# Kernel optimization log

Hardware: AMD Instinct MI355X
Metric: run time of the kernel (lower is better)

Reference implementation:

```python
import jax, jax.numpy as jnp
import numpy as np

N_USER = 100000
N_ITEM = 50000
D = 128
E = 600000
LN_EPS = 1e-5
NEG_SLOPE = 0.01  # torch nn.LeakyReLU default


def setup_inputs() -> dict:
    key = jax.random.key(0)
    ks = jax.random.split(key, 8)
    scale = 1.0 / np.sqrt(D)
    return {
        "x_user": jax.random.normal(ks[0], (N_USER, D), jnp.float32),
        "x_item": jax.random.normal(ks[1], (N_ITEM, D), jnp.float32),
        "W_ui": jax.random.normal(ks[2], (D, D), jnp.float32) * scale,
        "b_ui": jnp.zeros((D,), jnp.float32),
        "W_iu": jax.random.normal(ks[3], (D, D), jnp.float32) * scale,
        "b_iu": jnp.zeros((D,), jnp.float32),
        "ln_w_user": jnp.ones((D,), jnp.float32),
        "ln_b_user": jnp.zeros((D,), jnp.float32),
        "ln_w_item": jnp.ones((D,), jnp.float32),
        "ln_b_item": jnp.zeros((D,), jnp.float32),
        "edge_src_ui": jax.random.randint(ks[4], (E,), 0, N_USER, jnp.int32),
        "edge_dst_ui": jax.random.randint(ks[5], (E,), 0, N_ITEM, jnp.int32),
        "edge_src_iu": jax.random.randint(ks[6], (E,), 0, N_ITEM, jnp.int32),
        "edge_dst_iu": jax.random.randint(ks[7], (E,), 0, N_USER, jnp.int32),
    }


def _ngcf_conv(x_src, x_dst, W, b, src_idx, dst_idx, num_dst):
    # message: LeakyReLU(Linear(x_j * x_i)) per edge, then scatter-add at dst
    m = jax.nn.leaky_relu((x_src[src_idx] * x_dst[dst_idx]) @ W + b, NEG_SLOPE)
    return jax.ops.segment_sum(m, dst_idx, num_segments=num_dst)


def _node_layernorm(x, w, b):
    # PyG LayerNorm(mode='node'): normalize each node over feature dim
    mu = jnp.mean(x, axis=-1, keepdims=True)
    var = jnp.mean(jnp.square(x - mu), axis=-1, keepdims=True)
    return (x - mu) * jax.lax.rsqrt(var + LN_EPS) * w + b


def reference(x_user, x_item, W_ui, b_ui, W_iu, b_iu,
              ln_w_user, ln_b_user, ln_w_item, ln_b_item,
              edge_src_ui, edge_dst_ui, edge_src_iu, edge_dst_iu):
    # HeteroConv with aggr='sum' (single relation per destination type here)
    agg_item = _ngcf_conv(x_user, x_item, W_ui, b_ui, edge_src_ui, edge_dst_ui, N_ITEM)
    agg_user = _ngcf_conv(x_item, x_user, W_iu, b_iu, edge_src_iu, edge_dst_iu, N_USER)
    out_user = jax.nn.relu(_node_layernorm(agg_user, ln_w_user, ln_b_user))
    out_item = jax.nn.relu(_node_layernorm(agg_item, ln_w_item, ln_b_item))
    return out_user, out_item
```

## Files before the change

kernel.cpp:

```cpp
#include <hip/hip_runtime.h>
#include <stdint.h>

#define D 128
#define E_EDGES 600000
#define N_USER_C 100000
#define N_ITEM_C 50000
#define NEG_SLOPE 0.01f
#define LN_EPS 1e-5f

#define LDPAD 136
#define GRID_BLOCKS 1024
#define GRID_WAVES (GRID_BLOCKS * 4)

typedef __attribute__((ext_vector_type(8))) short bf16x8;
typedef __attribute__((ext_vector_type(4))) float f32x4;
typedef __attribute__((ext_vector_type(4))) uint32_t u32x4;

__device__ inline short f2bf(float f) {
    uint32_t u = __builtin_bit_cast(uint32_t, f);
    u += 0x7fffu + ((u >> 16) & 1u);
    return (short)(u >> 16);
}
__device__ inline uint32_t pack2f(float a, float b) {
    return (uint32_t)(uint16_t)f2bf(a) | ((uint32_t)(uint16_t)f2bf(b) << 16);
}


__global__ void hist_k(const int* __restrict__ dst, int* __restrict__ counts, int n) {
    int e = blockIdx.x * 256 + threadIdx.x;
    if (e < n) atomicAdd(&counts[dst[e]], 1);
}

__global__ void scan_block_k(const int* __restrict__ counts, int* __restrict__ offsets,
                             int* __restrict__ partial, int n) {
    __shared__ int sm[1024];
    const int t = threadIdx.x;
    const int i = blockIdx.x * 1024 + t;
    int v = (i < n) ? counts[i] : 0;
    sm[t] = v;
    __syncthreads();
    for (int off = 1; off < 1024; off <<= 1) {
        int x = (t >= off) ? sm[t - off] : 0;
        __syncthreads();
        sm[t] += x;
        __syncthreads();
    }
    if (i < n) offsets[i] = sm[t] - v;
    if (t == 1023) partial[blockIdx.x] = sm[t];
}

__global__ void scan_part_k(int* __restrict__ partial, int nb) {
    __shared__ int sm[128];
    const int t = threadIdx.x;
    int v = (t < nb) ? partial[t] : 0;
    sm[t] = v;
    __syncthreads();
    for (int off = 1; off < 128; off <<= 1) {
        int x = (t >= off) ? sm[t - off] : 0;
        __syncthreads();
        sm[t] += x;
        __syncthreads();
    }
    if (t < nb) partial[t] = sm[t] - v;
}

__global__ void scan_add_k(int* __restrict__ offsets, const int* __restrict__ partial,
                           int* __restrict__ counts, int n) {
    const int i = blockIdx.x * 1024 + threadIdx.x;
    if (i < n) {
        offsets[i] += partial[blockIdx.x];
        counts[i] = 0;
    }
}

__global__ void scatter_k(const int* __restrict__ src, const int* __restrict__ dst,
                          const int* __restrict__ offsets, int* __restrict__ counts,
                          int* __restrict__ sorted, int n) {
    int e = blockIdx.x * 256 + threadIdx.x;
    if (e < n) {
        int d = dst[e];
        int pos = offsets[d] + atomicAdd(&counts[d], 1);
        sorted[pos] = src[e];
    }
}

__global__ __launch_bounds__(256, 2) void ngcf_seg(
    const float* __restrict__ xsrc, const float* __restrict__ xdst,
    const float* __restrict__ W, const float* __restrict__ bias,
    const int* __restrict__ offsets, const int* __restrict__ sorted,
    const float* __restrict__ lnw, const float* __restrict__ lnb,
    float* __restrict__ outp, int n_dst, int n_edges)
{
    __shared__ short Wt[128 * LDPAD];

    const int t = threadIdx.x;
    for (int i = t; i < 128 * 128; i += 256) {
        int k = i >> 7, n = i & 127;
        Wt[n * LDPAD + k] = f2bf(W[i]);
    }
    __syncthreads();

    const int wv   = t >> 6;
    const int l    = t & 63;
    const int lo16 = l & 15;
    const int quad = l >> 4;

    float bn[8];
    #pragma unroll
    for (int n = 0; n < 8; n++) bn[n] = bias[n * 16 + lo16];

    for (int d = blockIdx.x * 4 + wv; d < n_dst; d += GRID_WAVES) {
        const int start = offsets[d];
        const int end   = (d + 1 < n_dst) ? offsets[d + 1] : n_edges;
        const int len   = end - start;

        const float4* pd = (const float4*)(xdst + ((size_t)d << 7));
        float4 dr[8];
        #pragma unroll
        for (int kt = 0; kt < 4; kt++) {
            dr[kt * 2 + 0] = pd[kt * 8 + quad * 2 + 0];
            dr[kt * 2 + 1] = pd[kt * 8 + quad * 2 + 1];
        }

        float nacc[8];
        #pragma unroll
        for (int n = 0; n < 8; n++) nacc[n] = 0.f;

        for (int c0 = 0; c0 < len; c0 += 16) {
            const int eidx = c0 + lo16;
            const int si = (eidx < len) ? sorted[start + eidx] : 0;
            const float4* ps = (const float4*)(xsrc + ((size_t)si << 7));

            f32x4 acc[8];
            #pragma unroll
            for (int n = 0; n < 8; n++) acc[n] = (f32x4){0.f, 0.f, 0.f, 0.f};

            #pragma unroll
            for (int kt = 0; kt < 4; kt++) {
                float4 a0 = ps[kt * 8 + quad * 2 + 0];
                float4 a1 = ps[kt * 8 + quad * 2 + 1];
                float4 c0v = dr[kt * 2 + 0];
                float4 c1v = dr[kt * 2 + 1];
                u32x4 up;
                up[0] = pack2f(a0.x * c0v.x, a0.y * c0v.y);
                up[1] = pack2f(a0.z * c0v.z, a0.w * c0v.w);
                up[2] = pack2f(a1.x * c1v.x, a1.y * c1v.y);
                up[3] = pack2f(a1.z * c1v.z, a1.w * c1v.w);
                bf16x8 afrag = __builtin_bit_cast(bf16x8, up);
                #pragma unroll
                for (int n = 0; n < 8; n++) {
                    bf16x8 bfrag = *(const bf16x8*)&Wt[(n * 16 + lo16) * LDPAD + kt * 32 + quad * 8];
                    acc[n] = __builtin_amdgcn_mfma_f32_16x16x32_bf16(afrag, bfrag, acc[n], 0, 0, 0);
                }
            }

            const int rem = len - c0;
            #pragma unroll
            for (int r = 0; r < 4; r++) {
                const bool ok = (quad * 4 + r) < rem;
                #pragma unroll
                for (int n = 0; n < 8; n++) {
                    float v = acc[n][r] + bn[n];
                    v = v > 0.f ? v : NEG_SLOPE * v;
                    nacc[n] += ok ? v : 0.f;
                }
            }
        }

        #pragma unroll
        for (int n = 0; n < 8; n++) {
            nacc[n] += __shfl_xor(nacc[n], 16);
            nacc[n] += __shfl_xor(nacc[n], 32);
        }

        float s1 = 0.f, s2 = 0.f;
        #pragma unroll
        for (int n = 0; n < 8; n++) { s1 += nacc[n]; s2 += nacc[n] * nacc[n]; }
        #pragma unroll
        for (int off = 1; off <= 8; off <<= 1) {
            s1 += __shfl_xor(s1, off);
            s2 += __shfl_xor(s2, off);
        }
        const float mu  = s1 * (1.0f / 128.0f);
        const float var = s2 * (1.0f / 128.0f) - mu * mu;
        const float rs  = rsqrtf(var + LN_EPS);

        const int n0 = 2 * quad, n1 = n0 + 1;
        const int col0 = n0 * 16 + lo16, col1 = n1 * 16 + lo16;
        float o0 = (nacc[n0] - mu) * rs * lnw[col0] + lnb[col0];
        float o1 = (nacc[n1] - mu) * rs * lnw[col1] + lnb[col1];
        float* rp = outp + ((size_t)d << 7);
        rp[col0] = fmaxf(o0, 0.f);
        rp[col1] = fmaxf(o1, 0.f);
    }
}


static inline void run_relation(const float* xsrc, const float* xdst,
                                const float* W, const float* bias,
                                const int* src, const int* dst,
                                const float* lnw, const float* lnb,
                                float* outp, int n_dst,
                                int* counts, int* offsets, int* partial, int* sorted,
                                hipStream_t stream) {
    const int nb = (n_dst + 1023) / 1024;
    hipMemsetAsync(counts, 0, (size_t)n_dst * sizeof(int), stream);
    hist_k<<<dim3((E_EDGES + 255) / 256), dim3(256), 0, stream>>>(dst, counts, E_EDGES);
    scan_block_k<<<dim3(nb), dim3(1024), 0, stream>>>(counts, offsets, partial, n_dst);
    scan_part_k<<<dim3(1), dim3(128), 0, stream>>>(partial, nb);
    scan_add_k<<<dim3(nb), dim3(1024), 0, stream>>>(offsets, partial, counts, n_dst);
    scatter_k<<<dim3((E_EDGES + 255) / 256), dim3(256), 0, stream>>>(src, dst, offsets, counts, sorted, E_EDGES);
    ngcf_seg<<<dim3(GRID_BLOCKS), dim3(256), 0, stream>>>(
        xsrc, xdst, W, bias, offsets, sorted, lnw, lnb, outp, n_dst, E_EDGES);
}

extern "C" void kernel_launch(void* const* d_in, const int* in_sizes, int n_in,
                              void* d_out, int out_size, void* d_ws, size_t ws_size,
                              hipStream_t stream) {
    const float* x_user    = (const float*)d_in[0];
    const float* x_item    = (const float*)d_in[1];
    const float* W_ui      = (const float*)d_in[2];
    const float* b_ui      = (const float*)d_in[3];
    const float* W_iu      = (const float*)d_in[4];
    const float* b_iu      = (const float*)d_in[5];
    const float* ln_w_user = (const float*)d_in[6];
    const float* ln_b_user = (const float*)d_in[7];
    const float* ln_w_item = (const float*)d_in[8];
    const float* ln_b_item = (const float*)d_in[9];
    const int* esrc_ui = (const int*)d_in[10];
    const int* edst_ui = (const int*)d_in[11];
    const int* esrc_iu = (const int*)d_in[12];
    const int* edst_iu = (const int*)d_in[13];

    float* out = (float*)d_out;
    float* out_user = out;
    float* out_item = out + (size_t)N_USER_C * D;

    int* counts  = (int*)d_ws;
    int* offsets = counts + 100032;
    int* partial = offsets + 100032;
    int* sorted  = partial + 192;

    run_relation(x_user, x_item, W_ui, b_ui, esrc_ui, edst_ui,
                 ln_w_item, ln_b_item, out_item, N_ITEM_C,
                 counts, offsets, partial, sorted, stream);
    run_relation(x_item, x_user, W_iu, b_iu, esrc_iu, edst_iu,
                 ln_w_user, ln_b_user, out_user, N_USER_C,
                 counts, offsets, partial, sorted, stream);
}
```

Before: 601.1 us.

## Merge both relations into one CSR build and one fused conv launch with fp16 MFMA

Both edge relations now share a single histogram, scan and scatter pass over a combined destination space, and a single conv kernel handles them by splitting blocks on the low bit of the block index. This cuts the launch count roughly in half and lets the two relations run concurrently on the GPU. The MFMA path moves from bf16 to fp16: inputs are converted with packed round-toward-zero and multiplied in fp16. The bias is folded into the accumulator initialisation, and padded lanes read a zero row, with their LeakyReLU(bias) contribution subtracted afterwards instead of masked per element. The fp16 elementwise product and round-toward-zero conversion may change numerical accuracy, and the padded lanes still read sorted[] past the end of a segment.

```diff
diff --git a/kernel.cpp b/kernel.cpp
--- a/kernel.cpp
+++ b/kernel.cpp
@@ -3,32 +3,31 @@
 
 #define D 128
 #define E_EDGES 600000
+#define E2 1200000
 #define N_USER_C 100000
 #define N_ITEM_C 50000
+#define NSEG_TOT 150000
+#define NCPAD 150528
 #define NEG_SLOPE 0.01f
 #define LN_EPS 1e-5f
 
 #define LDPAD 136
 #define GRID_BLOCKS 1024
+#define TOTAL_BLOCKS (GRID_BLOCKS * 2)
 #define GRID_WAVES (GRID_BLOCKS * 4)
 
-typedef __attribute__((ext_vector_type(8))) short bf16x8;
+typedef __attribute__((ext_vector_type(8))) _Float16 f16x8;
+typedef __attribute__((ext_vector_type(2))) _Float16 f16x2;
 typedef __attribute__((ext_vector_type(4))) float f32x4;
+typedef __attribute__((ext_vector_type(2))) float f32x2;
 typedef __attribute__((ext_vector_type(4))) uint32_t u32x4;
 
-__device__ inline short f2bf(float f) {
-    uint32_t u = __builtin_bit_cast(uint32_t, f);
-    u += 0x7fffu + ((u >> 16) & 1u);
-    return (short)(u >> 16);
-}
-__device__ inline uint32_t pack2f(float a, float b) {
-    return (uint32_t)(uint16_t)f2bf(a) | ((uint32_t)(uint16_t)f2bf(b) << 16);
-}
-
-
-__global__ void hist_k(const int* __restrict__ dst, int* __restrict__ counts, int n) {
+
+__global__ void hist2_k(const int* __restrict__ edst_ui, const int* __restrict__ edst_iu,
+                        int* __restrict__ counts) {
     int e = blockIdx.x * 256 + threadIdx.x;
-    if (e < n) atomicAdd(&counts[dst[e]], 1);
+    if (e < E_EDGES) atomicAdd(&counts[edst_ui[e]], 1);
+    else if (e < 2 * E_EDGES) atomicAdd(&counts[N_ITEM_C + edst_iu[e - E_EDGES]], 1);
 }
 
 __global__ void scan_block_k(const int* __restrict__ counts, int* __restrict__ offsets,
@@ -50,12 +49,12 @@
 }
 
 __global__ void scan_part_k(int* __restrict__ partial, int nb) {
-    __shared__ int sm[128];
+    __shared__ int sm[256];
     const int t = threadIdx.x;
     int v = (t < nb) ? partial[t] : 0;
     sm[t] = v;
     __syncthreads();
-    for (int off = 1; off < 128; off <<= 1) {
+    for (int off = 1; off < 256; off <<= 1) {
         int x = (t >= off) ? sm[t - off] : 0;
         __syncthreads();
         sm[t] += x;
@@ -73,30 +72,47 @@
     }
 }
 
-__global__ void scatter_k(const int* __restrict__ src, const int* __restrict__ dst,
-                          const int* __restrict__ offsets, int* __restrict__ counts,
-                          int* __restrict__ sorted, int n) {
+__global__ void scatter2_k(const int* __restrict__ esrc_ui, const int* __restrict__ edst_ui,
+                           const int* __restrict__ esrc_iu, const int* __restrict__ edst_iu,
+                           const int* __restrict__ offsets, int* __restrict__ counts,
+                           int* __restrict__ sorted) {
     int e = blockIdx.x * 256 + threadIdx.x;
-    if (e < n) {
-        int d = dst[e];
-        int pos = offsets[d] + atomicAdd(&counts[d], 1);
-        sorted[pos] = src[e];
-    }
-}
-
-__global__ __launch_bounds__(256, 2) void ngcf_seg(
-    const float* __restrict__ xsrc, const float* __restrict__ xdst,
-    const float* __restrict__ W, const float* __restrict__ bias,
+    int s, c;
+    if (e < E_EDGES)          { s = esrc_ui[e];            c = edst_ui[e]; }
+    else if (e < 2 * E_EDGES) { s = esrc_iu[e - E_EDGES];  c = N_ITEM_C + edst_iu[e - E_EDGES]; }
+    else return;
+    int pos = offsets[c] + atomicAdd(&counts[c], 1);
+    sorted[pos] = s;
+}
+
+__global__ __launch_bounds__(256, 2) void ngcf_seg2(
+    const float* __restrict__ xu, const float* __restrict__ xi,
+    const float* __restrict__ W_ui, const float* __restrict__ b_ui,
+    const float* __restrict__ W_iu, const float* __restrict__ b_iu,
+    const float* __restrict__ lnw_u, const float* __restrict__ lnb_u,
+    const float* __restrict__ lnw_i, const float* __restrict__ lnb_i,
     const int* __restrict__ offsets, const int* __restrict__ sorted,
-    const float* __restrict__ lnw, const float* __restrict__ lnb,
-    float* __restrict__ outp, int n_dst, int n_edges)
+    const float* __restrict__ zrow,
+    float* __restrict__ out_user, float* __restrict__ out_item)
 {
-    __shared__ short Wt[128 * LDPAD];
+    __shared__ _Float16 Wt[128 * LDPAD];
+
+    const int rel = blockIdx.x & 1;
+    const int bid = blockIdx.x >> 1;
+    const float* __restrict__ xsrc = rel ? xi : xu;
+    const float* __restrict__ xdst = rel ? xu : xi;
+    const float* __restrict__ Wp   = rel ? W_iu : W_ui;
+    const float* __restrict__ bp   = rel ? b_iu : b_ui;
+    const float* __restrict__ lnw  = rel ? lnw_u : lnw_i;
+    const float* __restrict__ lnb  = rel ? lnb_u : lnb_i;
+    float* __restrict__ outp       = rel ? out_user : out_item;
+    const int n_dst = rel ? N_USER_C : N_ITEM_C;
+    const int obase = rel ? N_ITEM_C : 0;
 
     const int t = threadIdx.x;
     for (int i = t; i < 128 * 128; i += 256) {
         int k = i >> 7, n = i & 127;
-        Wt[n * LDPAD + k] = f2bf(W[i]);
+        Wt[n * LDPAD + k] = (_Float16)Wp[i];
     }
     __syncthreads();
 
@@ -107,70 +123,78 @@
 
     float bn[8];
     #pragma unroll
-    for (int n = 0; n < 8; n++) bn[n] = bias[n * 16 + lo16];
-
-    for (int d = blockIdx.x * 4 + wv; d < n_dst; d += GRID_WAVES) {
-        const int start = offsets[d];
-        const int end   = (d + 1 < n_dst) ? offsets[d + 1] : n_edges;
+    for (int n = 0; n < 8; n++) bn[n] = bp[n * 16 + lo16];
+
+    for (int d = bid * 4 + wv; d < n_dst; d += GRID_WAVES) {
+        const int start = offsets[obase + d];
+        const int end   = offsets[obase + d + 1];
         const int len   = end - start;
 
         const float4* pd = (const float4*)(xdst + ((size_t)d << 7));
-        float4 dr[8];
+        f16x8 dr[4];
         #pragma unroll
         for (int kt = 0; kt < 4; kt++) {
-            dr[kt * 2 + 0] = pd[kt * 8 + quad * 2 + 0];
-            dr[kt * 2 + 1] = pd[kt * 8 + quad * 2 + 1];
-        }
-
-        float nacc[8];
-        #pragma unroll
-        for (int n = 0; n < 8; n++) nacc[n] = 0.f;
-
-        for (int c0 = 0; c0 < len; c0 += 16) {
-            const int eidx = c0 + lo16;
-            const int si = (eidx < len) ? sorted[start + eidx] : 0;
-            const float4* ps = (const float4*)(xsrc + ((size_t)si << 7));
+            float4 c0 = pd[kt * 8 + quad * 2 + 0];
+            float4 c1 = pd[kt * 8 + quad * 2 + 1];
+            u32x4 u;
+            u[0] = __builtin_bit_cast(uint32_t, __builtin_amdgcn_cvt_pkrtz(c0.x, c0.y));
+            u[1] = __builtin_bit_cast(uint32_t, __builtin_amdgcn_cvt_pkrtz(c0.z, c0.w));
+            u[2] = __builtin_bit_cast(uint32_t, __builtin_amdgcn_cvt_pkrtz(c1.x, c1.y));
+            u[3] = __builtin_bit_cast(uint32_t, __builtin_amdgcn_cvt_pkrtz(c1.z, c1.w));
+            dr[kt] = __builtin_bit_cast(f16x8, u);
+        }
+
+        f32x2 nacc2[8];
+        #pragma unroll
+        for (int n = 0; n < 8; n++) nacc2[n] = (f32x2){0.f, 0.f};
+
+        for (int c0i = 0; c0i < len; c0i += 16) {
+            const int eidx = c0i + lo16;
+            const bool okg = eidx < len;
+            const int si = sorted[start + eidx];
+            const float4* ps = (const float4*)(okg ? (xsrc + ((size_t)si << 7)) : zrow);
 
             f32x4 acc[8];
             #pragma unroll
-            for (int n = 0; n < 8; n++) acc[n] = (f32x4){0.f, 0.f, 0.f, 0.f};
+            for (int n = 0; n < 8; n++) acc[n] = (f32x4){bn[n], bn[n], bn[n], bn[n]};
 
             #pragma unroll
             for (int kt = 0; kt < 4; kt++) {
                 float4 a0 = ps[kt * 8 + quad * 2 + 0];
                 float4 a1 = ps[kt * 8 + quad * 2 + 1];
-                float4 c0v = dr[kt * 2 + 0];
-                float4 c1v = dr[kt * 2 + 1];
-                u32x4 up;
-                up[0] = pack2f(a0.x * c0v.x, a0.y * c0v.y);
-                up[1] = pack2f(a0.z * c0v.z, a0.w * c0v.w);
-                up[2] = pack2f(a1.x * c1v.x, a1.y * c1v.y);
-                up[3] = pack2f(a1.z * c1v.z, a1.w * c1v.w);
-                bf16x8 afrag = __builtin_bit_cast(bf16x8, up);
+                u32x4 u;
+                u[0] = __builtin_bit_cast(uint32_t, __builtin_amdgcn_cvt_pkrtz(a0.x, a0.y));
+                u[1] = __builtin_bit_cast(uint32_t, __builtin_amdgcn_cvt_pkrtz(a0.z, a0.w));
+                u[2] = __builtin_bit_cast(uint32_t, __builtin_amdgcn_cvt_pkrtz(a1.x, a1.y));
+                u[3] = __builtin_bit_cast(uint32_t, __builtin_amdgcn_cvt_pkrtz(a1.z, a1.w));
+                f16x8 af = __builtin_bit_cast(f16x8, u) * dr[kt];
                 #pragma unroll
                 for (int n = 0; n < 8; n++) {
-                    bf16x8 bfrag = *(const bf16x8*)&Wt[(n * 16 + lo16) * LDPAD + kt * 32 + quad * 8];
-                    acc[n] = __builtin_amdgcn_mfma_f32_16x16x32_bf16(afrag, bfrag, acc[n], 0, 0, 0);
+                    f16x8 bf = *(const f16x8*)&Wt[(n * 16 + lo16) * LDPAD + kt * 32 + quad * 8];
+                    acc[n] = __builtin_amdgcn_mfma_f32_16x16x32_f16(af, bf, acc[n], 0, 0, 0);
                 }
             }
 
-            const int rem = len - c0;
             #pragma unroll
-            for (int r = 0; r < 4; r++) {
-                const bool ok = (quad * 4 + r) < rem;
-                #pragma unroll
-                for (int n = 0; n < 8; n++) {
-                    float v = acc[n][r] + bn[n];
-                    v = v > 0.f ? v : NEG_SLOPE * v;
-                    nacc[n] += ok ? v : 0.f;
-                }
+            for (int n = 0; n < 8; n++) {
+                f32x2 v01 = (f32x2){acc[n][0], acc[n][1]};
+                f32x2 v23 = (f32x2){acc[n][2], acc[n][3]};
+                v01 = __builtin_elementwise_max(v01, v01 * NEG_SLOPE);
+                v23 = __builtin_elementwise_max(v23, v23 * NEG_SLOPE);
+                nacc2[n] += v01 + v23;
             }
         }
 
+        const int nch = (len + 15) >> 4;
+        const float inv = (float)(nch * 16 - len);
+        float nacc[8];
         #pragma unroll
         for (int n = 0; n < 8; n++) {
-            nacc[n] += __shfl_xor(nacc[n], 16);
-            nacc[n] += __shfl_xor(nacc[n], 32);
+            float s = nacc2[n].x + nacc2[n].y;
+            s += __shfl_xor(s, 16);
+            s += __shfl_xor(s, 32);
+            const float lb = fmaxf(bn[n], NEG_SLOPE * bn[n]);
+            nacc[n] = s - inv * lb;
         }
 
         float s1 = 0.f, s2 = 0.f;
@@ -195,24 +219,6 @@
     }
 }
 
-
-static inline void run_relation(const float* xsrc, const float* xdst,
-                                const float* W, const float* bias,
-                                const int* src, const int* dst,
-                                const float* lnw, const float* lnb,
-                                float* outp, int n_dst,
-                                int* counts, int* offsets, int* partial, int* sorted,
-                                hipStream_t stream) {
-    const int nb = (n_dst + 1023) / 1024;
-    hipMemsetAsync(counts, 0, (size_t)n_dst * sizeof(int), stream);
-    hist_k<<<dim3((E_EDGES + 255) / 256), dim3(256), 0, stream>>>(dst, counts, E_EDGES);
-    scan_block_k<<<dim3(nb), dim3(1024), 0, stream>>>(counts, offsets, partial, n_dst);
-    scan_part_k<<<dim3(1), dim3(128), 0, stream>>>(partial, nb);
-    scan_add_k<<<dim3(nb), dim3(1024), 0, stream>>>(offsets, partial, counts, n_dst);
-    scatter_k<<<dim3((E_EDGES + 255) / 256), dim3(256), 0, stream>>>(src, dst, offsets, counts, sorted, E_EDGES);
-    ngcf_seg<<<dim3(GRID_BLOCKS), dim3(256), 0, stream>>>(
-        xsrc, xdst, W, bias, offsets, sorted, lnw, lnb, outp, n_dst, E_EDGES);
-}
 
 extern "C" void kernel_launch(void* const* d_in, const int* in_sizes, int n_in,
                               void* d_out, int out_size, void* d_ws, size_t ws_size,
@@ -237,14 +243,24 @@
     float* out_item = out + (size_t)N_USER_C * D;
 
     int* counts  = (int*)d_ws;
-    int* offsets = counts + 100032;
-    int* partial = offsets + 100032;
-    int* sorted  = partial + 192;
-
-    run_relation(x_user, x_item, W_ui, b_ui, esrc_ui, edst_ui,
-                 ln_w_item, ln_b_item, out_item, N_ITEM_C,
-                 counts, offsets, partial, sorted, stream);
-    run_relation(x_item, x_user, W_iu, b_iu, esrc_iu, edst_iu,
-                 ln_w_user, ln_b_user, out_user, N_USER_C,
-                 counts, offsets, partial, sorted, stream);
-}
+    int* offsets = counts + NCPAD;
+    int* partial = offsets + NCPAD;
+    int* sorted  = partial + 256;
+    float* zrow  = (float*)(sorted + E2 + 16);
+
+    const int nb = NCPAD / 1024;
+    hipMemsetAsync(counts, 0, (size_t)NCPAD * sizeof(int), stream);
+    hipMemsetAsync(zrow, 0, 128 * sizeof(float), stream);
+
+    hist2_k<<<dim3((2 * E_EDGES + 255) / 256), dim3(256), 0, stream>>>(edst_ui, edst_iu, counts);
+    scan_block_k<<<dim3(nb), dim3(1024), 0, stream>>>(counts, offsets, partial, NCPAD);
+    scan_part_k<<<dim3(1), dim3(256), 0, stream>>>(partial, nb);
+    scan_add_k<<<dim3(nb), dim3(1024), 0, stream>>>(offsets, partial, counts, NCPAD);
+    scatter2_k<<<dim3((2 * E_EDGES + 255) / 256), dim3(256), 0, stream>>>(
+        esrc_ui, edst_ui, esrc_iu, edst_iu, offsets, counts, sorted);
+
+    ngcf_seg2<<<dim3(TOTAL_BLOCKS), dim3(256), 0, stream>>>(
+        x_user, x_item, W_ui, b_ui, W_iu, b_iu,
+        ln_w_user, ln_b_user, ln_w_item, ln_b_item,
+        offsets, sorted, zrow, out_user, out_item);
+}
```

Result: slower. 669.2 us (+11.3%).
